# Kernel optimization log

Measured on AMD Instinct MI355X. Metric: run time of the kernel, lower is better.

The kernel has to match this reference:

```python
import jax, jax.numpy as jnp
import numpy as np

BATCH, LENGTH, FEAT, RANK = 4096, 128, 4, 64
SCALE = 1.0 / np.sqrt(RANK)  # keep 128-step matrix chain numerically stable


def setup_inputs() -> dict:
    key = jax.random.key(0)
    k1, k2, k3, k4 = jax.random.split(key, 4)
    return {
        "input_data": jax.random.normal(k1, (BATCH, LENGTH, FEAT), dtype=jnp.float32),
        "first_core": jax.random.normal(k2, (FEAT, RANK), dtype=jnp.float32) * SCALE,
        "mid_cores": jax.random.normal(k3, (LENGTH - 2, RANK, FEAT, RANK), dtype=jnp.float32) * SCALE,
        "last_core": jax.random.normal(k4, (RANK, FEAT), dtype=jnp.float32) * SCALE,
    }


def reference(input_data, first_core, mid_cores, last_core):
    # input_data: [b, L, f] -> site-major [L, b, f]
    x = jnp.transpose(input_data, (1, 0, 2))
    # Per-site contraction with the physical (feature) index.
    v0 = jnp.einsum("ir,bi->br", first_core, x[0])            # [b, r]
    mid_mats = jnp.einsum("slir,sbi->sblr", mid_cores, x[1:-1])  # [S, b, r, r]
    last_vec = jnp.einsum("li,bi->bl", last_core, x[-1])      # [b, r]

    # Sequential tensor-train chain: v <- v @ M_s for each middle site.
    def step(v, mat):
        return jnp.einsum("bl,blr->br", v, mat), None

    v, _ = jax.lax.scan(step, v0, mid_mats)
    # Final contraction against last site vector -> [b, 1]
    out = jnp.sum(v * last_vec, axis=-1, keepdims=True)
    return out
```

## Files before the change

kernel.cpp:

```cpp
#include <hip/hip_runtime.h>
#include <stdint.h>

#define NSITES 126
#define XPITCH 516
#define VPH    72

typedef _Float16 half8_t  __attribute__((ext_vector_type(8)));
typedef float    float4_t __attribute__((ext_vector_type(4)));

#define LBAR() asm volatile("s_waitcnt lgkmcnt(0)\n\ts_barrier" ::: "memory")
#define WAITV(N) asm volatile("s_waitcnt vmcnt(" #N ")" ::: "memory")
#define TIE8(F) asm volatile("" : "+v"(F[0]), "+v"(F[1]), "+v"(F[2]), "+v"(F[3]), \
                                  "+v"(F[4]), "+v"(F[5]), "+v"(F[6]), "+v"(F[7]))

__device__ __forceinline__ void aload(half8_t& d, const void* p) {
    asm volatile("global_load_dwordx4 %0, %1, off" : "=v"(d) : "v"(p));
}

__global__ __launch_bounds__(256) void repack_g(const float* __restrict__ mid,
                                                _Float16* __restrict__ gt) {
    const int F = blockIdx.x * 256 + threadIdx.x;
    const int lane = F & 63, w = (F >> 6) & 3, h = (F >> 8) & 1, i = (F >> 9) & 3;
    const int s = F >> 11;
    const int q = lane >> 4, c = lane & 15;
    const float* src = mid + (size_t)s * 16384 + (32 * h + 8 * q) * 256 + i * 64 + w * 16 + c;
    half8_t o;
#pragma unroll
    for (int j = 0; j < 8; ++j) o[j] = (_Float16)src[j * 256];
    ((half8_t*)gt)[F] = o;
}

__global__ __launch_bounds__(256) void tt_chain(
    const float* __restrict__ x,
    const float* __restrict__ first,
    const float* __restrict__ last,
    const _Float16* __restrict__ gt,
    float* __restrict__ out) {

    __shared__ __align__(16) _Float16 vbuf[2][16 * VPH];
    __shared__ float xbuf[16 * XPITCH];
    __shared__ int   eacc[16];

    const int tid  = threadIdx.x;
    const int w    = tid >> 6;
    const int lane = tid & 63;
    const int q    = lane >> 4;
    const int c    = lane & 15;
    const int b0   = blockIdx.x * 16;

    {
        const int bb = tid >> 4, seg = tid & 15;
        const float4_t* src = (const float4_t*)(x + (size_t)(b0 + bb) * 512 + seg * 32);
        float4_t* dst = (float4_t*)(xbuf + bb * XPITCH + seg * 32);
#pragma unroll
        for (int k = 0; k < 8; ++k) dst[k] = src[k];
    }
    if (tid < 16) eacc[tid] = 0;
    __syncthreads();

    {
        const int bb = tid >> 4, rq = tid & 15;
        const float xs0 = xbuf[bb * XPITCH + 0], xs1 = xbuf[bb * XPITCH + 1];
        const float xs2 = xbuf[bb * XPITCH + 2], xs3 = xbuf[bb * XPITCH + 3];
#pragma unroll
        for (int k = 0; k < 4; ++k) {
            const int r = rq * 4 + k;
            vbuf[0][bb * VPH + r] = (_Float16)(
                xs0 * first[r] + xs1 * first[64 + r] + xs2 * first[128 + r] + xs3 * first[192 + r]);
        }
    }

    half8_t F0[8], F1[8], F2[8];
    const char* gbase = (const char*)gt + w * 1024 + lane * 16;
    auto LOAD = [&](int s, half8_t* F) {
        const char* p = gbase + (size_t)s * 32768;
#pragma unroll
        for (int ih = 0; ih < 8; ++ih) aload(F[ih], p + ih * 4096);
    };
    LOAD(0, F0);
    LOAD(1, F1);
    LBAR();

    auto STEP = [&](int s, half8_t* F) {
        const int p = s & 1;

        const _Float16* vr = &vbuf[p][c * VPH];
        half8_t af0 = *(const half8_t*)(vr + q * 8);
        half8_t af1 = *(const half8_t*)(vr + 32 + q * 8);
        float4_t xs[4];
#pragma unroll
        for (int jj = 0; jj < 4; ++jj)
            xs[jj] = *(const float4_t*)(xbuf + (q * 4 + jj) * XPITCH + (s + 1) * 4);

        WAITV(16);
        TIE8(F);

        if ((s & 7) == 0 && s != 0) {
            float a[16];
#pragma unroll
            for (int k = 0; k < 8; ++k) { a[k] = (float)af0[k]; a[8 + k] = (float)af1[k]; }
            float m = 0.f;
#pragma unroll
            for (int k = 0; k < 16; ++k) m = fmaxf(m, fabsf(a[k]));
            m = fmaxf(m, __shfl_xor(m, 16));
            m = fmaxf(m, __shfl_xor(m, 32));
            int e = 0;
            if (m > 0.f) frexpf(m, &e);
            const float sc = ldexpf(1.0f, -e);
#pragma unroll
            for (int k = 0; k < 8; ++k) {
                af0[k] = (_Float16)(a[k] * sc);
                af1[k] = (_Float16)(a[8 + k] * sc);
            }
            if (tid < 16) eacc[tid] += e;
        }

        float4_t acc[4];
#pragma unroll
        for (int i = 0; i < 4; ++i) {
            float4_t z = {0.f, 0.f, 0.f, 0.f};
            z = __builtin_amdgcn_mfma_f32_16x16x32_f16(af0, F[i * 2 + 0], z, 0, 0, 0);
            z = __builtin_amdgcn_mfma_f32_16x16x32_f16(af1, F[i * 2 + 1], z, 0, 0, 0);
            acc[i] = z;
        }

#pragma unroll
        for (int jj = 0; jj < 4; ++jj) {
            const float vn = xs[jj].x * acc[0][jj] + xs[jj].y * acc[1][jj] +
                             xs[jj].z * acc[2][jj] + xs[jj].w * acc[3][jj];
            vbuf[p ^ 1][(q * 4 + jj) * VPH + w * 16 + c] = (_Float16)vn;
        }
        LBAR();
    };

    for (int s = 0; s < NSITES; s += 3) {
        const int s2 = (s + 2 < NSITES) ? s + 2 : NSITES - 1;
        const int s3 = (s + 3 < NSITES) ? s + 3 : NSITES - 1;
        const int s4 = (s + 4 < NSITES) ? s + 4 : NSITES - 1;
        LOAD(s2, F2);
        STEP(s, F0);
        LOAD(s3, F0);
        STEP(s + 1, F1);
        LOAD(s4, F1);
        STEP(s + 2, F2);
    }
    WAITV(0);

    {
        const int bb = tid >> 4, rq = tid & 15;
        const float x0 = xbuf[bb * XPITCH + 508], x1 = xbuf[bb * XPITCH + 509];
        const float x2 = xbuf[bb * XPITCH + 510], x3 = xbuf[bb * XPITCH + 511];
        float dot = 0.f;
#pragma unroll
        for (int k = 0; k < 4; ++k) {
            const int r = rq * 4 + k;
            const float lv = last[r * 4 + 0] * x0 + last[r * 4 + 1] * x1 +
                             last[r * 4 + 2] * x2 + last[r * 4 + 3] * x3;
            dot += lv * (float)vbuf[0][bb * VPH + r];
        }
#pragma unroll
        for (int o = 8; o > 0; o >>= 1) dot += __shfl_xor(dot, o, 16);
        if (rq == 0) out[b0 + bb] = ldexpf(dot, eacc[bb]);
    }
}

extern "C" void kernel_launch(void* const* d_in, const int* in_sizes, int n_in,
                              void* d_out, int out_size, void* d_ws, size_t ws_size,
                              hipStream_t stream) {
    (void)in_sizes; (void)n_in; (void)out_size; (void)ws_size;
    const float* x     = (const float*)d_in[0];
    const float* first = (const float*)d_in[1];
    const float* mid   = (const float*)d_in[2];
    const float* last  = (const float*)d_in[3];
    float* out = (float*)d_out;
    _Float16* gt = (_Float16*)d_ws;

    repack_g<<<1008, 256, 0, stream>>>(mid, gt);
    tt_chain<<<256, 256, 0, stream>>>(x, first, last, gt, out);
}
```

Measured before the change: 120.8 us.

## Stage core matrices through an LDS ring via global_load_lds instead of registers

Replaces the register-resident triple-buffered prefetch of per-site core fragments with a 3-slot shared-memory ring filled by direct global-to-LDS loads. Each step reads its fragments back from LDS with ds_read_b128. The goal is to lower VGPR pressure and simplify the loop to one step per iteration. The cost is an extra LDS read per step on the serial chain's critical path, plus about 136KB of dynamic shared memory, which forces one block per CU.

```diff
diff --git a/kernel.cpp b/kernel.cpp
--- a/kernel.cpp
+++ b/kernel.cpp
@@ -5,16 +5,29 @@
 #define XPITCH 516
 #define VPH    72
 
+#define RING_B   98304
+#define XBUF_OFF 98304
+#define VBUF_OFF 131328
+#define EACC_OFF 135936
+#define SMEM_B   136000
+
 typedef _Float16 half8_t  __attribute__((ext_vector_type(8)));
 typedef float    float4_t __attribute__((ext_vector_type(4)));
 
 #define LBAR() asm volatile("s_waitcnt lgkmcnt(0)\n\ts_barrier" ::: "memory")
 #define WAITV(N) asm volatile("s_waitcnt vmcnt(" #N ")" ::: "memory")
-#define TIE8(F) asm volatile("" : "+v"(F[0]), "+v"(F[1]), "+v"(F[2]), "+v"(F[3]), \
-                                  "+v"(F[4]), "+v"(F[5]), "+v"(F[6]), "+v"(F[7]))
-
-__device__ __forceinline__ void aload(half8_t& d, const void* p) {
-    asm volatile("global_load_dwordx4 %0, %1, off" : "=v"(d) : "v"(p));
+#define WAITL()  asm volatile("s_waitcnt lgkmcnt(0)" ::: "memory")
+
+__device__ __forceinline__ void gstage16(const void* g, void* l) {
+    __builtin_amdgcn_global_load_lds(
+        (const __attribute__((address_space(1))) void*)g,
+        (__attribute__((address_space(3))) void*)l, 16, 0, 0);
+}
+__device__ __forceinline__ uint32_t lds_off(const void* p) {
+    return (uint32_t)(uintptr_t)(const __attribute__((address_space(3))) void*)p;
+}
+__device__ __forceinline__ void lread(half8_t& d, uint32_t base, int imm) {
+    asm volatile("ds_read_b128 %0, %1 offset:%c2" : "=v"(d) : "v"(base), "i"(imm));
 }
 
 __global__ __launch_bounds__(256) void repack_g(const float* __restrict__ mid,
@@ -30,19 +43,21 @@
     ((half8_t*)gt)[F] = o;
 }
 
-__global__ __launch_bounds__(256) void tt_chain(
+__global__ __launch_bounds__(256, 1) void tt_chain(
     const float* __restrict__ x,
     const float* __restrict__ first,
     const float* __restrict__ last,
     const _Float16* __restrict__ gt,
     float* __restrict__ out) {
 
-    __shared__ __align__(16) _Float16 vbuf[2][16 * VPH];
-    __shared__ float xbuf[16 * XPITCH];
-    __shared__ int   eacc[16];
+    extern __shared__ __align__(16) char smem[];
+    char*     ring = smem;
+    float*    xbuf = (float*)(smem + XBUF_OFF);
+    _Float16* vbuf = (_Float16*)(smem + VBUF_OFF);
+    int*      eacc = (int*)(smem + EACC_OFF);
 
     const int tid  = threadIdx.x;
-    const int w    = tid >> 6;
+    const int wv   = tid >> 6;
     const int lane = tid & 63;
     const int q    = lane >> 4;
     const int c    = lane & 15;
@@ -65,26 +80,30 @@
 #pragma unroll
         for (int k = 0; k < 4; ++k) {
             const int r = rq * 4 + k;
-            vbuf[0][bb * VPH + r] = (_Float16)(
+            vbuf[bb * VPH + r] = (_Float16)(
                 xs0 * first[r] + xs1 * first[64 + r] + xs2 * first[128 + r] + xs3 * first[192 + r]);
         }
     }
 
-    half8_t F0[8], F1[8], F2[8];
-    const char* gbase = (const char*)gt + w * 1024 + lane * 16;
-    auto LOAD = [&](int s, half8_t* F) {
-        const char* p = gbase + (size_t)s * 32768;
-#pragma unroll
-        for (int ih = 0; ih < 8; ++ih) aload(F[ih], p + ih * 4096);
+    WAITV(0);
+
+    const uint32_t ring0 = lds_off(ring);
+    auto ISSUE = [&](int site, int slot) {
+        const char* gp = (const char*)gt + (size_t)site * 32768 + wv * 1024 + lane * 16;
+        char* lp = ring + slot * 32768 + wv * 1024;
+#pragma unroll
+        for (int ih = 0; ih < 8; ++ih) gstage16(gp + ih * 4096, lp + ih * 4096);
     };
-    LOAD(0, F0);
-    LOAD(1, F1);
+
+    ISSUE(0, 0);
+    ISSUE(1, 1);
+    WAITV(8);
     LBAR();
 
-    auto STEP = [&](int s, half8_t* F) {
+    auto STEP = [&](int s, int slot) {
         const int p = s & 1;
 
-        const _Float16* vr = &vbuf[p][c * VPH];
+        const _Float16* vr = &vbuf[p * (16 * VPH) + c * VPH];
         half8_t af0 = *(const half8_t*)(vr + q * 8);
         half8_t af1 = *(const half8_t*)(vr + 32 + q * 8);
         float4_t xs[4];
@@ -92,8 +111,12 @@
         for (int jj = 0; jj < 4; ++jj)
             xs[jj] = *(const float4_t*)(xbuf + (q * 4 + jj) * XPITCH + (s + 1) * 4);
 
-        WAITV(16);
-        TIE8(F);
+        const uint32_t gb = ring0 + slot * 32768 + wv * 1024 + lane * 16;
+        half8_t g[8];
+#pragma unroll
+        for (int ih = 0; ih < 8; ++ih) lread(g[ih], gb, ih * 4096);
+        WAITL();
+        __builtin_amdgcn_sched_barrier(0);
 
         if ((s & 7) == 0 && s != 0) {
             float a[16];
@@ -119,8 +142,8 @@
 #pragma unroll
         for (int i = 0; i < 4; ++i) {
             float4_t z = {0.f, 0.f, 0.f, 0.f};
-            z = __builtin_amdgcn_mfma_f32_16x16x32_f16(af0, F[i * 2 + 0], z, 0, 0, 0);
-            z = __builtin_amdgcn_mfma_f32_16x16x32_f16(af1, F[i * 2 + 1], z, 0, 0, 0);
+            z = __builtin_amdgcn_mfma_f32_16x16x32_f16(af0, g[i * 2 + 0], z, 0, 0, 0);
+            z = __builtin_amdgcn_mfma_f32_16x16x32_f16(af1, g[i * 2 + 1], z, 0, 0, 0);
             acc[i] = z;
         }
 
@@ -128,21 +151,16 @@
         for (int jj = 0; jj < 4; ++jj) {
             const float vn = xs[jj].x * acc[0][jj] + xs[jj].y * acc[1][jj] +
                              xs[jj].z * acc[2][jj] + xs[jj].w * acc[3][jj];
-            vbuf[p ^ 1][(q * 4 + jj) * VPH + w * 16 + c] = (_Float16)vn;
-        }
+            vbuf[(p ^ 1) * (16 * VPH) + (q * 4 + jj) * VPH + wv * 16 + c] = (_Float16)vn;
+        }
+    };
+
+    for (int s = 0; s < NSITES; ++s) {
+        const int sn = (s + 2 < NSITES) ? s + 2 : NSITES - 1;
+        ISSUE(sn, (s + 2) % 3);
+        STEP(s, s % 3);
+        WAITV(8);
         LBAR();
-    };
-
-    for (int s = 0; s < NSITES; s += 3) {
-        const int s2 = (s + 2 < NSITES) ? s + 2 : NSITES - 1;
-        const int s3 = (s + 3 < NSITES) ? s + 3 : NSITES - 1;
-        const int s4 = (s + 4 < NSITES) ? s + 4 : NSITES - 1;
-        LOAD(s2, F2);
-        STEP(s, F0);
-        LOAD(s3, F0);
-        STEP(s + 1, F1);
-        LOAD(s4, F1);
-        STEP(s + 2, F2);
     }
     WAITV(0);
 
@@ -156,7 +174,7 @@
             const int r = rq * 4 + k;
             const float lv = last[r * 4 + 0] * x0 + last[r * 4 + 1] * x1 +
                              last[r * 4 + 2] * x2 + last[r * 4 + 3] * x3;
-            dot += lv * (float)vbuf[0][bb * VPH + r];
+            dot += lv * (float)vbuf[bb * VPH + r];
         }
 #pragma unroll
         for (int o = 8; o > 0; o >>= 1) dot += __shfl_xor(dot, o, 16);
@@ -175,6 +193,9 @@
     float* out = (float*)d_out;
     _Float16* gt = (_Float16*)d_ws;
 
+    hipFuncSetAttribute((const void*)tt_chain,
+                        hipFuncAttributeMaxDynamicSharedMemorySize, SMEM_B);
+
     repack_g<<<1008, 256, 0, stream>>>(mid, gt);
-    tt_chain<<<256, 256, 0, stream>>>(x, first, last, gt, out);
-}
+    tt_chain<<<256, 256, SMEM_B, stream>>>(x, first, last, gt, out);
+}
```

After: 144.5 us. 19.6% more time.
